# Kernel tuning notes

Hardware: AMD Instinct MI355X
Metric: run time of the kernel (lower is better)

## Reference

```python
import jax, jax.numpy as jnp
import numpy as np

D_MODEL = 1024
N_HEADS = 16
D_HEAD = D_MODEL // N_HEADS
SEQ_LEN = 4096
BATCH = 1
WINDOW = 256
NUM_RAND = 32
GLOBAL_TOKENS = (0,)


def _bigbird_mask(seq_len: int) -> jnp.ndarray:
    """Additive mask (0 = attend, -inf = blocked): global + sliding window + random.
    Random token selection is deterministic (fixed seed), mirroring torch.manual_seed(42)."""
    rng = np.random.default_rng(42)
    mask = np.full((seq_len, seq_len), -np.inf, dtype=np.float32)
    idx = np.arange(seq_len)
    # sliding window: |i-j| <= WINDOW (end = i + window + 1 in the original)
    band = np.abs(idx[:, None] - idx[None, :]) <= WINDOW
    mask[band] = 0.0
    # global tokens: full row + full column
    for g in GLOBAL_TOKENS:
        mask[g, :] = 0.0
        mask[:, g] = 0.0
    not_global = ~np.isin(idx, np.array(GLOBAL_TOKENS))
    gset = set(GLOBAL_TOKENS)
    for i in range(seq_len):
        if i in gset:
            continue
        cand = idx[(np.abs(idx - i) > WINDOW) & not_global]
        if cand.size >= NUM_RAND:
            sel = rng.choice(cand, size=NUM_RAND, replace=False)
            mask[i, sel] = 0.0
    return jnp.asarray(mask)


def setup_inputs() -> dict:
    key = jax.random.key(0)
    ks = jax.random.split(key, 9)
    s = 1.0 / np.sqrt(D_MODEL)
    x = jax.random.normal(ks[0], (BATCH, SEQ_LEN, D_MODEL), dtype=jnp.float32)
    # torch.nn.Linear weights are [out_features, in_features]
    Wq = jax.random.normal(ks[1], (D_MODEL, D_MODEL), dtype=jnp.float32) * s
    Wk = jax.random.normal(ks[2], (D_MODEL, D_MODEL), dtype=jnp.float32) * s
    Wv = jax.random.normal(ks[3], (D_MODEL, D_MODEL), dtype=jnp.float32) * s
    Wo = jax.random.normal(ks[4], (D_MODEL, D_MODEL), dtype=jnp.float32) * s
    bq = jax.random.normal(ks[5], (D_MODEL,), dtype=jnp.float32) * s
    bk = jax.random.normal(ks[6], (D_MODEL,), dtype=jnp.float32) * s
    bv = jax.random.normal(ks[7], (D_MODEL,), dtype=jnp.float32) * s
    bo = jax.random.normal(ks[8], (D_MODEL,), dtype=jnp.float32) * s
    mask = _bigbird_mask(SEQ_LEN)
    return {"x": x, "Wq": Wq, "bq": bq, "Wk": Wk, "bk": bk,
            "Wv": Wv, "bv": bv, "Wo": Wo, "bo": bo, "mask": mask}


def reference(x, Wq, bq, Wk, bk, Wv, bv, Wo, bo, mask):
    B, S, D = x.shape
    H, dh = N_HEADS, D_HEAD
    scale = dh ** -0.5
    q = (x @ Wq.T + bq).reshape(B, S, H, dh)  # [B,S,H,dh]
    k = (x @ Wk.T + bk).reshape(B, S, H, dh)
    v = (x @ Wv.T + bv).reshape(B, S, H, dh)
    scores = jnp.einsum("bihd,bjhd->bhij", q, k) * scale + mask  # [B,H,S,S]
    attn = jax.nn.softmax(scores, axis=-1)  # dropout is identity in eval mode
    out = jnp.einsum("bhij,bjhd->bihd", attn, v).reshape(B, S, D)
    return out @ Wo.T + bo
```

## Files before the change

### kernel.cpp

```cpp
#include <hip/hip_runtime.h>

typedef __attribute__((ext_vector_type(8))) short short8;
typedef __attribute__((ext_vector_type(8))) _Float16 half8;
typedef __attribute__((ext_vector_type(4))) float f32x4;
typedef __attribute__((ext_vector_type(4))) float float4v;
typedef __attribute__((ext_vector_type(4))) unsigned uint4v;

#define MFMA16(a, b, c) __builtin_amdgcn_mfma_f32_16x16x32_f16(a, b, c, 0, 0, 0)

static __device__ __forceinline__ short f2h(float f) {
  _Float16 h = (_Float16)f;
  short s;
  __builtin_memcpy(&s, &h, 2);
  return s;
}
static __device__ __forceinline__ float h2f(unsigned short u) {
  _Float16 h;
  __builtin_memcpy(&h, &u, 2);
  return (float)h;
}

__global__ __launch_bounds__(256) void k_bitmask(const float* __restrict__ mask,
                                                 unsigned long long* __restrict__ bmT) {
  int wid = blockIdx.x * 4 + (threadIdx.x >> 6);
  int lane = threadIdx.x & 63;
  int ct = wid & 63, r = wid >> 6;
  float v = mask[(size_t)r * 4096 + ct * 64 + lane];
  unsigned long long bal = __ballot(v == 0.0f);
  if (lane == 0) bmT[(size_t)ct * 4096 + r] = bal;
}

__global__ __launch_bounds__(256) void k_randidx(const unsigned long long* __restrict__ bmT,
                                                 unsigned short* __restrict__ ridx,
                                                 unsigned* __restrict__ cntR) {
  int r = blockIdx.x * 4 + (threadIdx.x >> 6);
  int lane = threadIdx.x & 63;
  if (r == 0) {
    if (lane < 32) ridx[lane] = 0;
    if (lane == 0) cntR[0] = 0;
    return;
  }
  int rb = r >> 6;
  bool excl = (lane == 0) || (lane >= rb - 4 && lane <= rb + 4);
  unsigned long long w64 = excl ? 0ull : bmT[(size_t)lane * 4096 + r];
  int cnt = __popcll(w64);
  int p = cnt;
#pragma unroll
  for (int off = 1; off < 64; off <<= 1) {
    int t = __shfl_up(p, off);
    if (lane >= off) p += t;
  }
  int base = p - cnt;
  int total = __shfl(p, 63);
  while (w64) {
    int b = __ffsll((unsigned long long)w64) - 1;
    ridx[(size_t)r * 32 + base] = (unsigned short)(lane * 64 + b);
    ++base;
    w64 &= w64 - 1;
  }
  for (int t = total + lane; t < 32; t += 64) ridx[(size_t)r * 32 + t] = 0;
  if (lane == 63) cntR[r] = (unsigned)p;
}

__global__ __launch_bounds__(256) void k_cvt(const float* __restrict__ src,
                                             short* __restrict__ dst, int n8) {
  int i = blockIdx.x * 256 + threadIdx.x;
  if (i >= n8) return;
  float4v a = ((const float4v*)src)[2 * i];
  float4v b = ((const float4v*)src)[2 * i + 1];
  short8 o;
#pragma unroll
  for (int j = 0; j < 4; ++j) {
    o[j] = f2h(a[j]);
    o[4 + j] = f2h(b[j]);
  }
  ((short8*)dst)[i] = o;
}

__global__ __launch_bounds__(256) void k_cvtw(const float* __restrict__ wq,
                                              const float* __restrict__ wk,
                                              const float* __restrict__ wv,
                                              const float* __restrict__ wo,
                                              short* __restrict__ dst) {
  int i = blockIdx.x * 256 + threadIdx.x;
  int row = i >> 7, c8 = i & 127;
  const float* src = row < 1024 ? wq + row * 1024
                   : row < 2048 ? wk + (row - 1024) * 1024
                   : row < 3072 ? wv + (row - 2048) * 1024
                                : wo + (row - 3072) * 1024;
  float4v a = ((const float4v*)src)[2 * c8];
  float4v b = ((const float4v*)src)[2 * c8 + 1];
  short8 o;
#pragma unroll
  for (int j = 0; j < 4; ++j) {
    o[j] = f2h(a[j]);
    o[4 + j] = f2h(b[j]);
  }
  ((short8*)dst)[i] = o;
}

template <int EPI>
__global__ __launch_bounds__(256) void k_gemm(const short* __restrict__ Ag,
                                              const short* __restrict__ Bg,
                                              const float* __restrict__ b0,
                                              const float* __restrict__ b1,
                                              const float* __restrict__ b2,
                                              short* __restrict__ outb,
                                              float* __restrict__ outf) {
  const int K = 1024;
  const int LDT = 72;
  __shared__ short Ah[128 * LDT];
  __shared__ short Bh[128 * LDT];
  int tid = threadIdx.x, lane = tid & 63, w = tid >> 6;
  int bm = blockIdx.x * 128, bn = blockIdx.y * 128;
  int wm = (w >> 1) * 64, wn = (w & 1) * 64;
  int arow = lane & 15, ag = lane >> 4;
  int srow = tid >> 3, sc = (tid & 7) * 8;
  f32x4 acc[4][4] = {};

  for (int k0 = 0; k0 < K; k0 += 64) {
    __syncthreads();
#pragma unroll
    for (int p = 0; p < 4; ++p) {
      int r = srow + p * 32;
      *(short8*)&Ah[r * LDT + sc] = *(const short8*)&Ag[(bm + r) * K + k0 + sc];
      *(short8*)&Bh[r * LDT + sc] = *(const short8*)&Bg[(bn + r) * K + k0 + sc];
    }
    __syncthreads();
#pragma unroll
    for (int kk = 0; kk < 64; kk += 32) {
      int ko = kk + ag * 8;
      half8 af[4], bf[4];
#pragma unroll
      for (int mi = 0; mi < 4; ++mi)
        af[mi] = *(const half8*)&Ah[(wm + mi * 16 + arow) * LDT + ko];
#pragma unroll
      for (int ni = 0; ni < 4; ++ni)
        bf[ni] = *(const half8*)&Bh[(wn + ni * 16 + arow) * LDT + ko];
#pragma unroll
      for (int mi = 0; mi < 4; ++mi)
#pragma unroll
        for (int ni = 0; ni < 4; ++ni)
          acc[mi][ni] = MFMA16(af[mi], bf[ni], acc[mi][ni]);
    }
  }
#pragma unroll
  for (int mi = 0; mi < 4; ++mi)
#pragma unroll
    for (int ni = 0; ni < 4; ++ni)
#pragma unroll
      for (int r = 0; r < 4; ++r) {
        int row = bm + wm + mi * 16 + ag * 4 + r;
        int col = bn + wn + ni * 16 + arow;
        float v = acc[mi][ni][r];
        if (EPI == 0) {
          int cl = col & 1023;
          const float* bp = col < 1024 ? b0 : col < 2048 ? b1 : b2;
          v += bp[cl];
          int head = cl >> 6, dh = col & 63, pr = col >> 10;
          outb[pr * (16 * 4096 * 64) + (head * 4096 + row) * 64 + dh] = f2h(v);
        } else {
          v += b0[col];
          outf[row * 1024 + col] = v;
        }
      }
}

#define QS2 0.18033688f

__global__ __launch_bounds__(256) void k_rand(const short* __restrict__ q,
                                              const short* __restrict__ k,
                                              const short* __restrict__ v,
                                              const unsigned short* __restrict__ ridx,
                                              const unsigned* __restrict__ cntR,
                                              float* __restrict__ RO,
                                              float* __restrict__ RL) {
  __shared__ float Pp[4][4][32];
  __shared__ unsigned Pc[4][4][32];
  __shared__ float R0o[4][64];
  __shared__ float R0l[4];
  int tid = threadIdx.x, lane = tid & 63, w = tid >> 6;
  int bid = blockIdx.x;

  if (bid < 4096) {
    int head = bid & 15, rg = bid >> 4;
    int rbase = rg * 16 + w * 4;
    int rw = lane >> 4;
    int cl = lane & 15;
    int row = rbase + rw;
    const short* kh = k + (size_t)head * 4096 * 64;
    const short* vh = v + (size_t)head * 4096 * 64;
    unsigned cnt = cntR[row];
    unsigned col0 = ridx[(size_t)row * 32 + cl];
    unsigned col1 = ridx[(size_t)row * 32 + 16 + cl];
    const uint4v* qp4 = (const uint4v*)(q + ((size_t)head * 4096 + row) * 64);
    const uint4v* k0 = (const uint4v*)(kh + (size_t)col0 * 64);
    const uint4v* k1 = (const uint4v*)(kh + (size_t)col1 * 64);
    float s0 = 0.f, s1 = 0.f;
#pragma unroll
    for (int i = 0; i < 8; ++i) {
      uint4v qv = qp4[i];
      uint4v a = k0[i];
      uint4v b = k1[i];
#pragma unroll
      for (int jj = 0; jj < 4; ++jj) {
        float qlo = h2f((unsigned short)(qv[jj] & 0xffffu));
        float qhi = h2f((unsigned short)(qv[jj] >> 16));
        s0 = fmaf(qlo, h2f((unsigned short)(a[jj] & 0xffffu)), s0);
        s0 = fmaf(qhi, h2f((unsigned short)(a[jj] >> 16)), s0);
        s1 = fmaf(qlo, h2f((unsigned short)(b[jj] & 0xffffu)), s1);
        s1 = fmaf(qhi, h2f((unsigned short)(b[jj] >> 16)), s1);
      }
    }
    float p0 = (cl < (int)cnt) ? exp2f(fmaf(s0, QS2, -32.f)) : 0.f;
    float p1 = (cl + 16 < (int)cnt) ? exp2f(fmaf(s1, QS2, -32.f)) : 0.f;
    float ls = p0 + p1;
#pragma unroll
    for (int off = 1; off < 16; off <<= 1) ls += __shfl_xor(ls, off, 16);
    Pp[w][rw][cl] = p0;
    Pp[w][rw][16 + cl] = p1;
    Pc[w][rw][cl] = col0;
    Pc[w][rw][16 + cl] = col1;
    if (cl == 0 && row != 0) RL[(size_t)head * 4096 + row] = ls;
    int h2 = lane >> 5, r2 = (lane >> 3) & 3, ch = lane & 7;
    float o[8] = {};
#pragma unroll
    for (int i = 0; i < 16; ++i) {
      int ci = h2 * 16 + i;
      float pp = Pp[w][r2][ci];
      unsigned cc = Pc[w][r2][ci];
      uint4v vv = *(const uint4v*)(vh + (size_t)cc * 64 + ch * 8);
#pragma unroll
      for (int jj = 0; jj < 4; ++jj) {
        o[2 * jj] = fmaf(pp, h2f((unsigned short)(vv[jj] & 0xffffu)), o[2 * jj]);
        o[2 * jj + 1] = fmaf(pp, h2f((unsigned short)(vv[jj] >> 16)), o[2 * jj + 1]);
      }
    }
#pragma unroll
    for (int jj = 0; jj < 8; ++jj) o[jj] += __shfl_xor(o[jj], 32);
    int row2 = rbase + r2;
    if (h2 == 0 && row2 != 0) {
      float4v a = {o[0], o[1], o[2], o[3]};
      float4v b = {o[4], o[5], o[6], o[7]};
      float* ro = RO + ((size_t)head * 4096 + row2) * 64 + ch * 8;
      *(float4v*)ro = a;
      *(float4v*)(ro + 4) = b;
    }
  } else {
    int head = bid - 4096;
    const short* kh = k + (size_t)head * 4096 * 64;
    const short* vh = v + (size_t)head * 4096 * 64;
    const uint4v* qp4 = (const uint4v*)(q + (size_t)head * 4096 * 64);
    uint4v qv[8];
#pragma unroll
    for (int i = 0; i < 8; ++i) qv[i] = qp4[i];
    float o[8] = {};
    float lacc = 0.f;
    int grp = lane >> 3, ch8 = lane & 7;
    float* Pw = (float*)Pp[w];
    for (int chk = w; chk < 59; chk += 4) {
      int cb = 320 + chk * 64;
      const uint4v* kp4 = (const uint4v*)(kh + (size_t)(cb + lane) * 64);
      float s2 = 0.f;
#pragma unroll
      for (int i = 0; i < 8; ++i) {
        uint4v kv = kp4[i];
#pragma unroll
        for (int jj = 0; jj < 4; ++jj) {
          s2 = fmaf(h2f((unsigned short)(qv[i][jj] & 0xffffu)),
                    h2f((unsigned short)(kv[jj] & 0xffffu)), s2);
          s2 = fmaf(h2f((unsigned short)(qv[i][jj] >> 16)),
                    h2f((unsigned short)(kv[jj] >> 16)), s2);
        }
      }
      float p = exp2f(fmaf(s2, QS2, -32.f));
      lacc += p;
      Pw[lane] = p;
#pragma unroll
      for (int i = 0; i < 8; ++i) {
        float pp = Pw[grp * 8 + i];
        uint4v vv = *(const uint4v*)(vh + (size_t)(cb + grp * 8 + i) * 64 + ch8 * 8);
#pragma unroll
        for (int jj = 0; jj < 4; ++jj) {
          o[2 * jj] = fmaf(pp, h2f((unsigned short)(vv[jj] & 0xffffu)), o[2 * jj]);
          o[2 * jj + 1] = fmaf(pp, h2f((unsigned short)(vv[jj] >> 16)), o[2 * jj + 1]);
        }
      }
    }
#pragma unroll
    for (int off = 8; off < 64; off <<= 1) {
#pragma unroll
      for (int jj = 0; jj < 8; ++jj) o[jj] += __shfl_xor(o[jj], off);
      lacc += __shfl_xor(lacc, off);
    }
    lacc += __shfl_xor(lacc, 1);
    lacc += __shfl_xor(lacc, 2);
    lacc += __shfl_xor(lacc, 4);
    if (grp == 0) {
#pragma unroll
      for (int jj = 0; jj < 8; ++jj) R0o[w][ch8 * 8 + jj] = o[jj];
    }
    if (lane == 0) R0l[w] = lacc;
    __syncthreads();
    if (w == 0) {
      float o4 = R0o[0][lane] + R0o[1][lane] + R0o[2][lane] + R0o[3][lane];
      RO[(size_t)head * 4096 * 64 + lane] = o4;
      if (lane == 0) RL[(size_t)head * 4096] = R0l[0] + R0l[1] + R0l[2] + R0l[3];
    }
  }
}

__global__ __launch_bounds__(256) void k_flash(const short* __restrict__ q,
                                               const short* __restrict__ k,
                                               const short* __restrict__ v,
                                               const unsigned long long* __restrict__ bmT,
                                               const float* __restrict__ RO,
                                               const float* __restrict__ RL,
                                               short* __restrict__ ao) {
  const int LDT = 88;
  const int LDP = 72;
  __shared__ short Kl[64 * LDT];
  __shared__ short VT[64 * LDT];
  __shared__ short Pl[4 * 16 * LDP];
  __shared__ unsigned long long BM[64];
  int tid = threadIdx.x, lane = tid & 63, w = tid >> 6;
  int head = blockIdx.x & 15, rb = blockIdx.x >> 4;
  int q0 = rb * 64;
  int arow = lane & 15, ag = lane >> 4;
  int srow = tid >> 3, sc = (tid & 7) * 8;

  const short* qh = q + ((size_t)head * 4096 + q0 + w * 16) * 64;
  const short* kh = k + (size_t)head * 4096 * 64;
  const short* vh = v + (size_t)head * 4096 * 64;
  half8 aq0 = *(const half8*)&qh[arow * 64 + ag * 8];
  half8 aq1 = *(const half8*)&qh[arow * 64 + 32 + ag * 8];

  f32x4 accO[4] = {};
  float m[4] = {-1e30f, -1e30f, -1e30f, -1e30f};
  float lsum[4] = {0.f, 0.f, 0.f, 0.f};

  int t_lo = rb - 4; if (t_lo < 0) t_lo = 0;
  int t_hi = rb + 4; if (t_hi > 63) t_hi = 63;
  int extra0 = (t_lo > 0) ? 1 : 0;
  int nt = t_hi - t_lo + 1 + extra0;

  for (int it = 0; it < nt; ++it) {
    int ct = (extra0 && it == 0) ? 0 : t_lo + it - extra0;
    __syncthreads();
#pragma unroll
    for (int p = 0; p < 2; ++p) {
      int r = srow + p * 32;
      *(short8*)&Kl[r * LDT + sc] = *(const short8*)&kh[(ct * 64 + r) * 64 + sc];
    }
#pragma unroll
    for (int p = 0; p < 2; ++p) {
      int r = srow + p * 32;
      short8 vv = *(const short8*)&vh[(ct * 64 + r) * 64 + sc];
#pragma unroll
      for (int i = 0; i < 8; ++i) {
        int row = sc + i;
        VT[row * LDT + (r ^ (((row >> 3) & 7) << 3))] = vv[i];
      }
    }
    if (tid < 128)
      ((unsigned*)BM)[tid] = ((const unsigned*)(bmT + (size_t)ct * 4096 + q0))[tid];
    __syncthreads();

    f32x4 s[4];
    __builtin_amdgcn_s_setprio(1);
#pragma unroll
    for (int ni = 0; ni < 4; ++ni) {
      half8 b0 = *(const half8*)&Kl[(ni * 16 + arow) * LDT + ag * 8];
      half8 b1 = *(const half8*)&Kl[(ni * 16 + arow) * LDT + 32 + ag * 8];
      f32x4 z = {};
      z = MFMA16(aq0, b0, z);
      z = MFMA16(aq1, b1, z);
      s[ni] = z;
    }
    __builtin_amdgcn_s_setprio(0);
    float pv[4][4], mx[4];
#pragma unroll
    for (int r = 0; r < 4; ++r) {
      unsigned long long wrd = BM[w * 16 + ag * 4 + r];
      unsigned wlo = (unsigned)wrd, whi = (unsigned)(wrd >> 32);
      float rm = -1e30f;
#pragma unroll
      for (int ni = 0; ni < 4; ++ni) {
        unsigned word = (ni < 2) ? wlo : whi;
        unsigned bit = (word >> (arow + (ni & 1) * 16)) & 1u;
        float sv = s[ni][r] * QS2;
        sv = bit ? sv : -1e30f;
        pv[ni][r] = sv;
        rm = fmaxf(rm, sv);
      }
      mx[r] = rm;
    }
#pragma unroll
    for (int off = 1; off < 16; off <<= 1)
#pragma unroll
      for (int r = 0; r < 4; ++r) mx[r] = fmaxf(mx[r], __shfl_xor(mx[r], off, 16));
#pragma unroll
    for (int r = 0; r < 4; ++r) {
      float mnew = fmaxf(m[r], mx[r]);
      float alpha = exp2f(m[r] - mnew);
      m[r] = mnew;
      lsum[r] *= alpha;
      accO[0][r] *= alpha; accO[1][r] *= alpha;
      accO[2][r] *= alpha; accO[3][r] *= alpha;
      float rs = 0.f;
#pragma unroll
      for (int ni = 0; ni < 4; ++ni) {
        float p = exp2f(pv[ni][r] - mnew);
        pv[ni][r] = p;
        rs += p;
      }
#pragma unroll
      for (int off = 1; off < 16; off <<= 1) rs += __shfl_xor(rs, off, 16);
      lsum[r] += rs;
    }
    short* Pw = &Pl[w * 16 * LDP];
#pragma unroll
    for (int r = 0; r < 4; ++r)
#pragma unroll
      for (int ni = 0; ni < 4; ++ni)
        Pw[(ag * 4 + r) * LDP + ni * 16 + arow] = f2h(pv[ni][r]);
    __builtin_amdgcn_s_setprio(1);
#pragma unroll
    for (int kk2 = 0; kk2 < 2; ++kk2) {
      half8 pa = *(const half8*)&Pw[arow * LDP + kk2 * 32 + ag * 8];
#pragma unroll
      for (int f = 0; f < 4; ++f) {
        int drow = f * 16 + arow;
        int jo = (kk2 * 32 + ag * 8) ^ (((drow >> 3) & 7) << 3);
        half8 vb = *(const half8*)&VT[drow * LDT + jo];
        accO[f] = MFMA16(pa, vb, accO[f]);
      }
    }
    __builtin_amdgcn_s_setprio(0);
  }

#pragma unroll
  for (int r = 0; r < 4; ++r) {
    int rr = ag * 4 + r;
    int row = q0 + w * 16 + rr;
    float mF = fmaxf(m[r], 32.0f);
    float ab = exp2f(m[r] - mF);
    float aR = exp2f(32.0f - mF);
    float lR = RL[(size_t)head * 4096 + row];
    float lt = lsum[r] * ab + lR * aR;
#pragma unroll
    for (int f = 0; f < 4; ++f) {
      float o = accO[f][r] * ab + RO[((size_t)head * 4096 + row) * 64 + f * 16 + arow] * aR;
      o /= lt;
      ao[(size_t)row * 1024 + head * 64 + f * 16 + arow] = f2h(o);
    }
  }
}

extern "C" void kernel_launch(void* const* d_in, const int* in_sizes, int n_in,
                              void* d_out, int out_size, void* d_ws, size_t ws_size,
                              hipStream_t stream) {
  const float* x = (const float*)d_in[0];
  const float* Wq = (const float*)d_in[1];
  const float* bq = (const float*)d_in[2];
  const float* Wk = (const float*)d_in[3];
  const float* bk = (const float*)d_in[4];
  const float* Wv = (const float*)d_in[5];
  const float* bv = (const float*)d_in[6];
  const float* Wo = (const float*)d_in[7];
  const float* bo = (const float*)d_in[8];
  const float* mask = (const float*)d_in[9];

  char* ws = (char*)d_ws;
  unsigned long long* bmT = (unsigned long long*)(ws + 0);
  short* xh  = (short*)(ws + 2097152);
  short* wh  = (short*)(ws + 10485760);
  short* qkv = (short*)(ws + 18874368);
  unsigned short* ridx = (unsigned short*)(ws + 44040192);
  unsigned* cntR = (unsigned*)(ws + 44302336);
  float* RO = (float*)(ws + 44318720);
  float* RL = (float*)(ws + 61095936);
  short* ao = xh;
  const int QSZ = 16 * 4096 * 64;
  float* outf = (float*)d_out;

  k_bitmask<<<dim3(65536), dim3(256), 0, stream>>>(mask, bmT);
  k_randidx<<<dim3(1024), dim3(256), 0, stream>>>(bmT, ridx, cntR);
  k_cvt<<<dim3(2048), dim3(256), 0, stream>>>(x, xh, 524288);
  k_cvtw<<<dim3(2048), dim3(256), 0, stream>>>(Wq, Wk, Wv, Wo, wh);
  k_gemm<0><<<dim3(32, 24), dim3(256), 0, stream>>>(
      xh, wh, bq, bk, bv, qkv, nullptr);
  k_rand<<<dim3(4112), dim3(256), 0, stream>>>(qkv, qkv + QSZ, qkv + 2 * QSZ,
                                               ridx, cntR, RO, RL);
  k_flash<<<dim3(1024), dim3(256), 0, stream>>>(qkv, qkv + QSZ, qkv + 2 * QSZ, bmT,
                                                RO, RL, ao);
  k_gemm<1><<<dim3(32, 8), dim3(256), 0, stream>>>(
      ao, wh + 3072 * 1024, bo, nullptr, nullptr, nullptr, outf);
}
```

Measured before the change: 336.1 us.

## Restructure random-key attention so lanes split head dim, looping rows per wave

The random-attention part of k_rand now assigns each lane a 16-byte chunk of the head dimension for one of 8 candidate columns. Partial dot products are reduced with shuffles, and each wave loops over 8 rows instead of handling 4. The K and V gathers become coalesced 128-byte row reads, and the shared-memory staging of probabilities and column indices is removed. The grid is halved to 2064 blocks, so each block does more serial work and uses many more shuffles, which may lower latency hiding.

```diff
diff --git a/kernel.cpp b/kernel.cpp
--- a/kernel.cpp
+++ b/kernel.cpp
@@ -175,79 +175,71 @@
                                               const unsigned* __restrict__ cntR,
                                               float* __restrict__ RO,
                                               float* __restrict__ RL) {
-  __shared__ float Pp[4][4][32];
-  __shared__ unsigned Pc[4][4][32];
+  __shared__ float Pw0[4][64];
   __shared__ float R0o[4][64];
   __shared__ float R0l[4];
   int tid = threadIdx.x, lane = tid & 63, w = tid >> 6;
   int bid = blockIdx.x;
 
-  if (bid < 4096) {
+  if (bid < 2048) {
     int head = bid & 15, rg = bid >> 4;
-    int rbase = rg * 16 + w * 4;
-    int rw = lane >> 4;
-    int cl = lane & 15;
-    int row = rbase + rw;
+    int c_slot = lane >> 3, chunk = lane & 7;
     const short* kh = k + (size_t)head * 4096 * 64;
     const short* vh = v + (size_t)head * 4096 * 64;
-    unsigned cnt = cntR[row];
-    unsigned col0 = ridx[(size_t)row * 32 + cl];
-    unsigned col1 = ridx[(size_t)row * 32 + 16 + cl];
-    const uint4v* qp4 = (const uint4v*)(q + ((size_t)head * 4096 + row) * 64);
-    const uint4v* k0 = (const uint4v*)(kh + (size_t)col0 * 64);
-    const uint4v* k1 = (const uint4v*)(kh + (size_t)col1 * 64);
-    float s0 = 0.f, s1 = 0.f;
-#pragma unroll
-    for (int i = 0; i < 8; ++i) {
-      uint4v qv = qp4[i];
-      uint4v a = k0[i];
-      uint4v b = k1[i];
-#pragma unroll
-      for (int jj = 0; jj < 4; ++jj) {
-        float qlo = h2f((unsigned short)(qv[jj] & 0xffffu));
-        float qhi = h2f((unsigned short)(qv[jj] >> 16));
-        s0 = fmaf(qlo, h2f((unsigned short)(a[jj] & 0xffffu)), s0);
-        s0 = fmaf(qhi, h2f((unsigned short)(a[jj] >> 16)), s0);
-        s1 = fmaf(qlo, h2f((unsigned short)(b[jj] & 0xffffu)), s1);
-        s1 = fmaf(qhi, h2f((unsigned short)(b[jj] >> 16)), s1);
-      }
-    }
-    float p0 = (cl < (int)cnt) ? exp2f(fmaf(s0, QS2, -32.f)) : 0.f;
-    float p1 = (cl + 16 < (int)cnt) ? exp2f(fmaf(s1, QS2, -32.f)) : 0.f;
-    float ls = p0 + p1;
-#pragma unroll
-    for (int off = 1; off < 16; off <<= 1) ls += __shfl_xor(ls, off, 16);
-    Pp[w][rw][cl] = p0;
-    Pp[w][rw][16 + cl] = p1;
-    Pc[w][rw][cl] = col0;
-    Pc[w][rw][16 + cl] = col1;
-    if (cl == 0 && row != 0) RL[(size_t)head * 4096 + row] = ls;
-    int h2 = lane >> 5, r2 = (lane >> 3) & 3, ch = lane & 7;
-    float o[8] = {};
-#pragma unroll
-    for (int i = 0; i < 16; ++i) {
-      int ci = h2 * 16 + i;
-      float pp = Pp[w][r2][ci];
-      unsigned cc = Pc[w][r2][ci];
-      uint4v vv = *(const uint4v*)(vh + (size_t)cc * 64 + ch * 8);
-#pragma unroll
-      for (int jj = 0; jj < 4; ++jj) {
-        o[2 * jj] = fmaf(pp, h2f((unsigned short)(vv[jj] & 0xffffu)), o[2 * jj]);
-        o[2 * jj + 1] = fmaf(pp, h2f((unsigned short)(vv[jj] >> 16)), o[2 * jj + 1]);
-      }
-    }
-#pragma unroll
-    for (int jj = 0; jj < 8; ++jj) o[jj] += __shfl_xor(o[jj], 32);
-    int row2 = rbase + r2;
-    if (h2 == 0 && row2 != 0) {
-      float4v a = {o[0], o[1], o[2], o[3]};
-      float4v b = {o[4], o[5], o[6], o[7]};
-      float* ro = RO + ((size_t)head * 4096 + row2) * 64 + ch * 8;
-      *(float4v*)ro = a;
-      *(float4v*)(ro + 4) = b;
+    for (int rr = 0; rr < 8; ++rr) {
+      int row = rg * 32 + w * 8 + rr;
+      unsigned cnt = cntR[row];
+      uint4v qv = *(const uint4v*)(q + ((size_t)head * 4096 + row) * 64 + chunk * 8);
+      float qf[8];
+#pragma unroll
+      for (int j = 0; j < 4; ++j) {
+        qf[2 * j] = h2f((unsigned short)(qv[j] & 0xffffu));
+        qf[2 * j + 1] = h2f((unsigned short)(qv[j] >> 16));
+      }
+      float o8[8] = {};
+      float ls = 0.f;
+#pragma unroll
+      for (int pass = 0; pass < 4; ++pass) {
+        int ci = pass * 8 + c_slot;
+        unsigned col = ridx[(size_t)row * 32 + ci];
+        uint4v kv = *(const uint4v*)(kh + (size_t)col * 64 + chunk * 8);
+        float s = 0.f;
+#pragma unroll
+        for (int j = 0; j < 4; ++j) {
+          s = fmaf(qf[2 * j], h2f((unsigned short)(kv[j] & 0xffffu)), s);
+          s = fmaf(qf[2 * j + 1], h2f((unsigned short)(kv[j] >> 16)), s);
+        }
+        s += __shfl_xor(s, 1);
+        s += __shfl_xor(s, 2);
+        s += __shfl_xor(s, 4);
+        float p = (ci < (int)cnt) ? exp2f(fmaf(s, QS2, -32.f)) : 0.f;
+        ls += p;
+        uint4v vv = *(const uint4v*)(vh + (size_t)col * 64 + chunk * 8);
+#pragma unroll
+        for (int j = 0; j < 4; ++j) {
+          o8[2 * j] = fmaf(p, h2f((unsigned short)(vv[j] & 0xffffu)), o8[2 * j]);
+          o8[2 * j + 1] = fmaf(p, h2f((unsigned short)(vv[j] >> 16)), o8[2 * j + 1]);
+        }
+      }
+#pragma unroll
+      for (int off = 8; off < 64; off <<= 1) {
+#pragma unroll
+        for (int j = 0; j < 8; ++j) o8[j] += __shfl_xor(o8[j], off);
+        ls += __shfl_xor(ls, off);
+      }
+      if (row != 0) {
+        if (c_slot == 0) {
+          float4v a = {o8[0], o8[1], o8[2], o8[3]};
+          float4v b = {o8[4], o8[5], o8[6], o8[7]};
+          float* ro = RO + ((size_t)head * 4096 + row) * 64 + chunk * 8;
+          *(float4v*)ro = a;
+          *(float4v*)(ro + 4) = b;
+        }
+        if (lane == 0) RL[(size_t)head * 4096 + row] = ls;
+      }
     }
   } else {
-    int head = bid - 4096;
+    int head = bid - 2048;
     const short* kh = k + (size_t)head * 4096 * 64;
     const short* vh = v + (size_t)head * 4096 * 64;
     const uint4v* qp4 = (const uint4v*)(q + (size_t)head * 4096 * 64);
@@ -257,7 +249,7 @@
     float o[8] = {};
     float lacc = 0.f;
     int grp = lane >> 3, ch8 = lane & 7;
-    float* Pw = (float*)Pp[w];
+    float* Pw = Pw0[w];
     for (int chk = w; chk < 59; chk += 4) {
       int cb = 320 + chk * 64;
       const uint4v* kp4 = (const uint4v*)(kh + (size_t)(cb + lane) * 64);
@@ -490,7 +482,7 @@
   k_cvtw<<<dim3(2048), dim3(256), 0, stream>>>(Wq, Wk, Wv, Wo, wh);
   k_gemm<0><<<dim3(32, 24), dim3(256), 0, stream>>>(
       xh, wh, bq, bk, bv, qkv, nullptr);
-  k_rand<<<dim3(4112), dim3(256), 0, stream>>>(qkv, qkv + QSZ, qkv + 2 * QSZ,
+  k_rand<<<dim3(2064), dim3(256), 0, stream>>>(qkv, qkv + QSZ, qkv + 2 * QSZ,
                                                ridx, cntR, RO, RL);
   k_flash<<<dim3(1024), dim3(256), 0, stream>>>(qkv, qkv + QSZ, qkv + 2 * QSZ, bmT,
                                                 RO, RL, ao);
```

Measured after the change: 331.5 us. About the same (-1.4%).
